# Performance work log

Hardware: AMD Instinct MI355X
Metric: run time of the kernel (lower is better)

The kernel has to match this reference:

```python
import jax, jax.numpy as jnp
import numpy as np
from jax import lax

WINDOW_SIZE = 11
SIGMA = 1.5
C1 = 0.01 ** 2
C2 = 0.03 ** 2


def _gaussian_window(channels):
    coords = jnp.arange(WINDOW_SIZE, dtype=jnp.float32) - WINDOW_SIZE // 2
    g = jnp.exp(-coords ** 2 / (2.0 * SIGMA ** 2))
    g = g / g.sum()
    w2d = g[:, None] * g[None, :]  # [ws, ws]
    # depthwise kernel [C, 1, ws, ws] (OIHW with feature_group_count=C)
    return jnp.broadcast_to(w2d[None, None], (channels, 1, WINDOW_SIZE, WINDOW_SIZE))


def _depthwise_conv(x, window):
    pad = WINDOW_SIZE // 2
    return lax.conv_general_dilated(
        x, window,
        window_strides=(1, 1),
        padding=[(pad, pad), (pad, pad)],
        dimension_numbers=('NCHW', 'OIHW', 'NCHW'),
        feature_group_count=x.shape[1],
    )


def setup_inputs() -> dict:
    key = jax.random.key(0)
    k1, k2 = jax.random.split(key)
    shape = (4, 31, 512, 512)
    pred = jax.random.uniform(k1, shape, dtype=jnp.float32)
    target = jax.random.uniform(k2, shape, dtype=jnp.float32)
    return {"pred": pred, "target": target}


def reference(pred, target):
    C = pred.shape[1]
    window = _gaussian_window(C)

    mu_pred = _depthwise_conv(pred, window)
    mu_target = _depthwise_conv(target, window)
    mu_pred_sq = mu_pred ** 2
    mu_target_sq = mu_target ** 2
    mu_cross = mu_pred * mu_target

    sigma_pred_sq = _depthwise_conv(pred ** 2, window) - mu_pred_sq
    sigma_target_sq = _depthwise_conv(target ** 2, window) - mu_target_sq
    sigma_cross = _depthwise_conv(pred * target, window) - mu_cross

    sigma_pred_sq = jnp.clip(sigma_pred_sq, 0.0)
    sigma_target_sq = jnp.clip(sigma_target_sq, 0.0)

    ssim_map = ((2.0 * mu_cross + C1) * (2.0 * sigma_cross + C2)) / (
        (mu_pred_sq + mu_target_sq + C1) * (sigma_pred_sq + sigma_target_sq + C2)
    )
    return 1.0 - ssim_map.mean()
```

## Files before the change

### kernel.cpp

```cpp
#include <hip/hip_runtime.h>
#include <math.h>

#define HH 512
#define WW 512
#define HB 64
#define KR 4
#define SUB 138
#define ROWF4 (4 * SUB)


typedef float v2f __attribute__((ext_vector_type(2)));

__global__ __launch_bounds__(512, 1)
void ssim_main(const float* __restrict__ Pg, const float* __restrict__ Tg,
               float* __restrict__ partial) {
  __shared__ __align__(16) float4 S4[KR * ROWF4];
  __shared__ float wsum[8];

  const int tid = threadIdx.x;
  const int blk = blockIdx.x;
  const int plane = blk >> 3;
  const int band  = blk & 7;
  const int o0 = band * HB;
  const float* __restrict__ P = Pg + (size_t)plane * (HH * WW);
  const float* __restrict__ T = Tg + (size_t)plane * (HH * WW);

  {
    const float4 z = make_float4(0.f, 0.f, 0.f, 0.f);
    for (int idx = tid; idx < KR * ROWF4; idx += 512) S4[idx] = z;
  }

  float w[11];
  {
    double g[11], s = 0.0;
#pragma unroll
    for (int k = 0; k < 11; ++k) {
      double c = (double)(k - 5);
      g[k] = exp(-c * c / 4.5);
      s += g[k];
    }
#pragma unroll
    for (int k = 0; k < 11; ++k)
      w[k] = __uint_as_float(__builtin_amdgcn_readfirstlane(
                 __float_as_uint((float)(g[k] / s))));
  }

  float sum = 0.f;
  const int jr = tid >> 7;
  const int q  = tid & 127;
  float4* const rdbase = &S4[jr * ROWF4 + q + 2];
  float4* const wrbase = &S4[(tid & 3) * SUB + (tid >> 2) + 2];

  for (int g = 0; g < HB; g += KR) {
    v2f apt[KR], asq[KR];
    {
      const v2f z = {0.f, 0.f};
#pragma unroll
      for (int j = 0; j < KR; ++j) { apt[j] = z; asq[j] = z; }
    }
    const int rbase = o0 + g - 5;

#define VACC(RI, PV, TV) {                                                 \
      const float p_ = (PV), t_ = (TV);                                   \
      const v2f pt  = {p_, t_};                                           \
      const v2f q23 = {fmaf(t_, t_, p_ * p_), p_ * t_};                   \
      _Pragma("unroll")                                                   \
      for (int j = 0; j < KR; ++j) {                                      \
        if ((RI) - j >= 0 && (RI) - j <= 10) {                            \
          const float wk = w[(RI) - j];                                   \
          const v2f wv = {wk, wk};                                        \
          apt[j] = __builtin_elementwise_fma(wv, pt,  apt[j]);            \
          asq[j] = __builtin_elementwise_fma(wv, q23, asq[j]);            \
        }                                                                 \
      }                                                                   \
    }

    if (rbase >= 0 && rbase + 13 < HH) {
      const float* const Pr = P + (size_t)rbase * WW + tid;
      const float* const Tr = T + (size_t)rbase * WW + tid;
#pragma unroll
      for (int ri = 0; ri < KR + 10; ++ri) {
        VACC(ri, Pr[ri * WW], Tr[ri * WW]);
        if (ri == 6) __builtin_amdgcn_sched_barrier(0);
      }
    } else {
#pragma unroll
      for (int ri = 0; ri < KR + 10; ++ri) {
        const int r_in = rbase + ri;
        const bool v = (r_in >= 0) && (r_in < HH);
        const float p = v ? P[(size_t)r_in * WW + tid] : 0.f;
        const float t = v ? T[(size_t)r_in * WW + tid] : 0.f;
        VACC(ri, p, t);
        if (ri == 6) __builtin_amdgcn_sched_barrier(0);
      }
    }
#undef VACC

    __syncthreads();
#pragma unroll
    for (int j = 0; j < KR; ++j)
      wrbase[j * ROWF4] = make_float4(apt[j][0], apt[j][1], asq[j][0], asq[j][1]);
    __syncthreads();

    v2f hpt[4], hsq[4];
    {
      const v2f z = {0.f, 0.f};
#pragma unroll
      for (int m = 0; m < 4; ++m) { hpt[m] = z; hsq[m] = z; }
    }
#pragma unroll
    for (int k = 0; k < 14; ++k) {
      const int d = k - 5;
      const int s = d & 3;
      const int o = (d - s) >> 2;
      const float4 v4 = rdbase[s * SUB + o];
      const v2f lo = {v4.x, v4.y};
      const v2f hi = {v4.z, v4.w};
#pragma unroll
      for (int m = 0; m < 4; ++m) {
        if (k - m >= 0 && k - m <= 10) {
          const float wk = w[k - m];
          const v2f wv = {wk, wk};
          hpt[m] = __builtin_elementwise_fma(wv, lo, hpt[m]);
          hsq[m] = __builtin_elementwise_fma(wv, hi, hsq[m]);
        }
      }
      if (k == 6) __builtin_amdgcn_sched_barrier(0);
    }
#pragma unroll
    for (int m = 0; m < 4; ++m) {
      const float hmp = hpt[m][0], hmt = hpt[m][1];
      const float mp2 = hmp * hmp, mt2 = hmt * hmt, mct = hmp * hmt;
      const float ssum = fmaxf(hsq[m][0] - mp2 - mt2, 0.f);
      const float scv = hsq[m][1] - mct;
      const float num = fmaf(2.f, mct, 1.0e-4f) * fmaf(2.f, scv, 9.0e-4f);
      const float den = (mp2 + mt2 + 1.0e-4f) * (ssum + 9.0e-4f);
      sum += num * __builtin_amdgcn_rcpf(den);
    }
  }

#pragma unroll
  for (int off = 32; off > 0; off >>= 1) sum += __shfl_down(sum, off, 64);
  if ((tid & 63) == 0) wsum[tid >> 6] = sum;
  __syncthreads();
  if (tid == 0) {
    float s = 0.f;
#pragma unroll
    for (int k2 = 0; k2 < 8; ++k2) s += wsum[k2];
    partial[blk] = s;
  }
}

__global__ void ssim_fin(const float* __restrict__ partial,
                         float* __restrict__ out, int n) {
  __shared__ double ws[4];
  double s = 0.0;
  for (int idx = threadIdx.x; idx < n; idx += 256) s += (double)partial[idx];
#pragma unroll
  for (int off = 32; off > 0; off >>= 1) s += __shfl_down(s, off, 64);
  if ((threadIdx.x & 63) == 0) ws[threadIdx.x >> 6] = s;
  __syncthreads();
  if (threadIdx.x == 0) {
    double tt = ws[0] + ws[1] + ws[2] + ws[3];
    out[0] = (float)(1.0 - tt / 32505856.0);
  }
}

extern "C" void kernel_launch(void* const* d_in, const int* in_sizes, int n_in,
                              void* d_out, int out_size, void* d_ws, size_t ws_size,
                              hipStream_t stream) {
  const float* pred = (const float*)d_in[0];
  const float* tgt  = (const float*)d_in[1];
  float* out        = (float*)d_out;
  float* partial    = (float*)d_ws;

  ssim_main<<<dim3(992), dim3(512), 0, stream>>>(pred, tgt, partial);
  ssim_fin<<<dim3(1), dim3(256), 0, stream>>>(partial, out, 992);
}
```

Before: 112.5 us.

## Keep sliding row window in registers and prefetch next rows during compute

Instead of reloading all 14 input rows per 4-row group from global memory, the kernel keeps a 10-row register window, shifts it, and issues loads for the next 4 rows before the LDS horizontal pass, so global latency overlaps with compute. This cuts redundant global/L2 reads by about 3.5x per group. The __syncthreads calls are also replaced by barriers that wait only on LDS counters, so the in-flight global prefetches are not drained at each barrier. The cost is higher register pressure from the extra live values.

```diff
diff --git a/kernel.cpp b/kernel.cpp
--- a/kernel.cpp
+++ b/kernel.cpp
@@ -10,6 +10,12 @@
 
 
 typedef float v2f __attribute__((ext_vector_type(2)));
+
+__device__ __forceinline__ void bar_lgkm() {
+  asm volatile("s_waitcnt lgkmcnt(0)" ::: "memory");
+  __builtin_amdgcn_s_barrier();
+  __builtin_amdgcn_sched_barrier(0);
+}
 
 __global__ __launch_bounds__(512, 1)
 void ssim_main(const float* __restrict__ Pg, const float* __restrict__ Tg,
@@ -51,6 +57,21 @@
   float4* const rdbase = &S4[jr * ROWF4 + q + 2];
   float4* const wrbase = &S4[(tid & 3) * SUB + (tid >> 2) + 2];
 
+  float pr[10], tr[10], pn[4], tn[4];
+#pragma unroll
+  for (int i = 0; i < 10; ++i) {
+    const int r = o0 - 5 + i;
+    const bool v = (r >= 0);
+    pr[i] = v ? P[(size_t)r * WW + tid] : 0.f;
+    tr[i] = v ? T[(size_t)r * WW + tid] : 0.f;
+  }
+#pragma unroll
+  for (int i = 0; i < 4; ++i) {
+    const int r = o0 + 5 + i;
+    pn[i] = P[(size_t)r * WW + tid];
+    tn[i] = T[(size_t)r * WW + tid];
+  }
+
   for (int g = 0; g < HB; g += KR) {
     v2f apt[KR], asq[KR];
     {
@@ -58,7 +79,6 @@
 #pragma unroll
       for (int j = 0; j < KR; ++j) { apt[j] = z; asq[j] = z; }
     }
-    const int rbase = o0 + g - 5;
 
 #define VACC(RI, PV, TV) {                                                 \
       const float p_ = (PV), t_ = (TV);                                   \
@@ -75,32 +95,32 @@
       }                                                                   \
     }
 
-    if (rbase >= 0 && rbase + 13 < HH) {
-      const float* const Pr = P + (size_t)rbase * WW + tid;
-      const float* const Tr = T + (size_t)rbase * WW + tid;
 #pragma unroll
-      for (int ri = 0; ri < KR + 10; ++ri) {
-        VACC(ri, Pr[ri * WW], Tr[ri * WW]);
-        if (ri == 6) __builtin_amdgcn_sched_barrier(0);
-      }
-    } else {
+    for (int ri = 0; ri < 10; ++ri) VACC(ri, pr[ri], tr[ri]);
 #pragma unroll
-      for (int ri = 0; ri < KR + 10; ++ri) {
-        const int r_in = rbase + ri;
-        const bool v = (r_in >= 0) && (r_in < HH);
-        const float p = v ? P[(size_t)r_in * WW + tid] : 0.f;
-        const float t = v ? T[(size_t)r_in * WW + tid] : 0.f;
-        VACC(ri, p, t);
-        if (ri == 6) __builtin_amdgcn_sched_barrier(0);
+    for (int i = 0; i < 4; ++i) VACC(10 + i, pn[i], tn[i]);
+#undef VACC
+
+#pragma unroll
+    for (int i = 0; i < 6; ++i) { pr[i] = pr[i + 4]; tr[i] = tr[i + 4]; }
+#pragma unroll
+    for (int i = 0; i < 4; ++i) { pr[6 + i] = pn[i]; tr[6 + i] = tn[i]; }
+#pragma unroll
+    for (int i = 0; i < 4; ++i) {
+      const int r = o0 + g + 9 + i;
+      if (r < HH) {
+        pn[i] = P[(size_t)r * WW + tid];
+        tn[i] = T[(size_t)r * WW + tid];
+      } else {
+        pn[i] = 0.f; tn[i] = 0.f;
       }
     }
-#undef VACC
 
-    __syncthreads();
+    bar_lgkm();
 #pragma unroll
     for (int j = 0; j < KR; ++j)
       wrbase[j * ROWF4] = make_float4(apt[j][0], apt[j][1], asq[j][0], asq[j][1]);
-    __syncthreads();
+    bar_lgkm();
 
     v2f hpt[4], hsq[4];
     {
```

After: 101.3 us. 1.11x faster.
